# Kernel optimization log

Hardware: AMD Instinct MI355X
Metric: run time of the kernel (lower is better)

The kernel has to match this reference:

```python
import jax, jax.numpy as jnp
import numpy as np

N_NODES = 50000
N_EDGES = 1600000  # even; edges come in reverse pairs (i, i^1)
D_NODE = 128
D_EDGE = 32
UNITS = 128
STEPS = 4


def setup_inputs() -> dict:
    key = jax.random.key(0)
    ks = jax.random.split(key, 8)
    # Build directed edges as adjacent reverse pairs so rev(e) = e XOR 1.
    half = N_EDGES // 2
    src = jax.random.randint(ks[0], (half,), 0, N_NODES, dtype=jnp.int32)
    dst = jax.random.randint(ks[1], (half,), 0, N_NODES, dtype=jnp.int32)
    edge_src = jnp.stack([src, dst], axis=1).reshape(-1)
    edge_dst = jnp.stack([dst, src], axis=1).reshape(-1)
    node_feature = jax.random.normal(ks[2], (N_NODES, D_NODE), dtype=jnp.float32)
    edge_feature = jax.random.normal(ks[3], (N_EDGES, D_EDGE), dtype=jnp.float32)
    s_i = 1.0 / np.sqrt(D_NODE + D_EDGE)
    s_u = 1.0 / np.sqrt(UNITS)
    s_f = 1.0 / np.sqrt(D_NODE + UNITS)
    Wi = jax.random.normal(ks[4], (D_NODE + D_EDGE, UNITS), dtype=jnp.float32) * s_i
    Wu = jax.random.normal(ks[5], (UNITS, UNITS), dtype=jnp.float32) * s_u
    Wf = jax.random.normal(ks[6], (D_NODE + UNITS, UNITS), dtype=jnp.float32) * s_f
    bi = jnp.zeros((UNITS,), jnp.float32)
    bu = jnp.zeros((UNITS,), jnp.float32)
    bf = jnp.zeros((UNITS,), jnp.float32)
    return {
        'node_feature': node_feature, 'edge_feature': edge_feature,
        'edge_src': edge_src, 'edge_dst': edge_dst,
        'Wi': Wi, 'bi': bi, 'Wu': Wu, 'bu': bu, 'Wf': Wf, 'bf': bf,
    }


def reference(node_feature, edge_feature, edge_src, edge_dst, Wi, bi, Wu, bu, Wf, bf):
    n_nodes = node_feature.shape[0]
    n_edges = edge_src.shape[0]
    # reverse edge of e is e XOR 1 (edges built as adjacent pairs)
    rev = jnp.bitwise_xor(jnp.arange(n_edges, dtype=jnp.int32), 1)

    # initial projection: relu([x_src || e] Wi + bi)  -> [E, UNITS]
    h = jax.nn.relu(
        jnp.concatenate([node_feature[edge_src], edge_feature], axis=-1) @ Wi + bi)

    for _ in range(STEPS):
        # aggregate incoming edge states at each node, gather at edge_src,
        # subtract the reverse edge state (DMPNN message)
        agg = jax.ops.segment_sum(h, edge_dst, num_segments=n_nodes)  # [N, UNITS]
        message = agg[edge_src] - h[rev]                              # [E, UNITS]
        h = jax.nn.relu(message @ Wu + bu + h)

    node_message = jax.ops.segment_sum(h, edge_dst, num_segments=n_nodes)
    out = jax.nn.relu(
        jnp.concatenate([node_feature, node_message], axis=-1) @ Wf + bf)
    return out
```

## Files before the change

kernel.cpp:

```cpp
#include <hip/hip_runtime.h>
#include <hip/hip_bf16.h>

#define N_NODES 50000
#define N_EDGES 1600000
#define TILE    128

typedef __bf16 bf16x8 __attribute__((ext_vector_type(8)));
typedef __bf16 bf16x4 __attribute__((ext_vector_type(4)));
typedef float  f32x4  __attribute__((ext_vector_type(4)));

static __device__ __forceinline__ bf16x8 ld8(const __bf16* p) {
  return *reinterpret_cast<const bf16x8*>(p);
}
static __device__ __forceinline__ void st8(__bf16* p, bf16x8 v) {
  *reinterpret_cast<bf16x8*>(p) = v;
}

static __device__ __forceinline__ void async16(const void* g, void* l) {
  auto gp = (const __attribute__((address_space(1))) unsigned int*)(unsigned long long)g;
  auto lp = (__attribute__((address_space(3))) unsigned int*)(unsigned int)(unsigned long long)l;
  __builtin_amdgcn_global_load_lds(gp, lp, 16, 0, 0);
}

__global__ __launch_bounds__(256) void k_prep_w(
    const float* __restrict__ Wi, const float* __restrict__ Wu,
    const float* __restrict__ Wf,
    __bf16* __restrict__ WiT, __bf16* __restrict__ WuT, __bf16* __restrict__ WfT)
{
  int g = blockIdx.x * 256 + threadIdx.x;
  if (g < 160 * 128) {
    int n = g / 160, k = g % 160;
    WiT[g] = (__bf16)Wi[k * 128 + n];
  } else if (g < 160 * 128 + 128 * 128) {
    int gg = g - 160 * 128;
    int n = gg / 128, k = gg % 128;
    WuT[gg] = (__bf16)Wu[k * 128 + n];
  } else if (g < 160 * 128 + 128 * 128 + 256 * 128) {
    int gg = g - (160 * 128 + 128 * 128);
    int n = gg / 256, k = gg % 256;
    WfT[gg] = (__bf16)Wf[k * 128 + n];
  }
}

__global__ __launch_bounds__(256) void k_cvt(
    const float* __restrict__ in, __bf16* __restrict__ out, long n)
{
  long i = ((long)blockIdx.x * 256 + threadIdx.x) * 8;
  if (i + 8 <= n) {
    f32x4 f0 = *(const f32x4*)(in + i);
    f32x4 f1 = *(const f32x4*)(in + i + 4);
    bf16x8 o;
#pragma unroll
    for (int j = 0; j < 4; ++j) { o[j] = (__bf16)f0[j]; o[4 + j] = (__bf16)f1[j]; }
    st8(out + i, o);
  }
}

__global__ __launch_bounds__(256) void k_hist(
    const int* __restrict__ edst, int* __restrict__ cnt)
{
  int e = blockIdx.x * 256 + threadIdx.x;
  if (e < N_EDGES) atomicAdd(&cnt[edst[e]], 1);
}

__global__ __launch_bounds__(1024) void k_scan1(
    int* __restrict__ cnt, int* __restrict__ bsum, int n)
{
  __shared__ int sm[1024];
  const int tid = threadIdx.x;
  int i = blockIdx.x * 1024 + tid;
  int v = (i < n) ? cnt[i] : 0;
  sm[tid] = v;
  __syncthreads();
  for (int off = 1; off < 1024; off <<= 1) {
    int t = (tid >= off) ? sm[tid - off] : 0;
    __syncthreads();
    sm[tid] += t;
    __syncthreads();
  }
  if (i < n) cnt[i] = sm[tid] - v;
  if (tid == 1023) bsum[blockIdx.x] = sm[1023];
}

__global__ __launch_bounds__(64) void k_scan2(int* __restrict__ bsum, int nb)
{
  if (threadIdx.x == 0) {
    int acc = 0;
    for (int k = 0; k < nb; ++k) { int t = bsum[k]; bsum[k] = acc; acc += t; }
  }
}

__global__ __launch_bounds__(256) void k_scan3(
    const int* __restrict__ cnt, const int* __restrict__ bsum,
    int* __restrict__ cursor, int n)
{
  int i = blockIdx.x * 256 + threadIdx.x;
  if (i < n) cursor[i] = cnt[i] + bsum[i >> 10];
}

__global__ __launch_bounds__(256) void k_fill(
    const int* __restrict__ edst, int* __restrict__ cursor, int* __restrict__ eidx)
{
  int e = blockIdx.x * 256 + threadIdx.x;
  if (e < N_EDGES) {
    int p = atomicAdd(&cursor[edst[e]], 1);
    eidx[p] = e;
  }
}

__global__ __launch_bounds__(256) void k_agg(
    const __bf16* __restrict__ h, const int* __restrict__ cnt,
    const int* __restrict__ bsum, const int* __restrict__ eidx,
    const __bf16* __restrict__ zrow, __bf16* __restrict__ aggbf)
{
  const int wave = threadIdx.x >> 6;
  const int node = blockIdx.x * 4 + wave;
  const int lane = threadIdx.x & 63;
  const int g = lane >> 3, c8 = lane & 7;
  const int s = cnt[node] + bsum[node >> 10];
  const int e = (node + 1 < N_NODES) ? (cnt[node + 1] + bsum[(node + 1) >> 10]) : N_EDGES;
  const int deg = e - s;

  float a[16] = {};
  if (deg > 0) {
    const int* bucket = eidx + s;
    const int nit = (deg + 7) >> 3;
    int j0 = g;
    int e0 = bucket[(j0 < deg) ? j0 : 0];
    int e1 = bucket[(j0 + 8 < deg) ? j0 + 8 : 0];
    bool v0 = (j0 < deg), v1 = (j0 + 8 < deg);
    const __bf16* p0 = v0 ? (h + (long)e0 * 128 + c8 * 16) : zrow;
    bf16x8 r0 = ld8(p0), r1 = ld8(p0 + 8);
    for (int it = 0; it < nit; ++it) {
      const int j2 = j0 + 16;
      const int e2 = bucket[(j2 < deg) ? j2 : 0];
      const __bf16* p1 = v1 ? (h + (long)e1 * 128 + c8 * 16) : zrow;
      bf16x8 n0 = ld8(p1), n1 = ld8(p1 + 8);
#pragma unroll
      for (int k = 0; k < 8; ++k) {
        a[k]     += (float)r0[k];
        a[8 + k] += (float)r1[k];
      }
      r0 = n0; r1 = n1;
      e1 = e2; v1 = (j2 < deg);
      j0 += 8;
    }
  }
#pragma unroll
  for (int k = 0; k < 16; ++k) {
    a[k] += __shfl_xor(a[k], 8, 64);
    a[k] += __shfl_xor(a[k], 16, 64);
    a[k] += __shfl_xor(a[k], 32, 64);
  }
  if (g == 0) {
    bf16x8 o0, o1;
#pragma unroll
    for (int k = 0; k < 8; ++k) { o0[k] = (__bf16)a[k]; o1[k] = (__bf16)a[8 + k]; }
    st8(aggbf + (long)node * 128 + c8 * 16, o0);
    st8(aggbf + (long)node * 128 + c8 * 16 + 8, o1);
  }
}

__global__ __launch_bounds__(256) void k_nodegemm(
    const __bf16* __restrict__ A, const __bf16* __restrict__ BT, const int ldb,
    const float* __restrict__ bias, __bf16* __restrict__ outb, const int nrows)
{
  const int tid = threadIdx.x;
  const int lane = tid & 63, wave = tid >> 6;
  const int l15 = lane & 15, quad = lane >> 4;
  const int wm = wave >> 1, wn = wave & 1;
  const int base = blockIdx.x * TILE;

  int rowm[4];
#pragma unroll
  for (int ms = 0; ms < 4; ++ms) {
    int nd = base + wm * 64 + ms * 16 + l15;
    rowm[ms] = nd < nrows ? nd : (nrows - 1);
  }
  f32x4 acc[4][4] = {};
#pragma unroll
  for (int kit = 0; kit < 4; ++kit) {
    const int koff = kit * 32 + quad * 8;
    bf16x8 b[4];
#pragma unroll
    for (int ms = 0; ms < 4; ++ms)
      b[ms] = ld8(A + (long)rowm[ms] * 128 + koff);
#pragma unroll
    for (int ns = 0; ns < 4; ++ns) {
      bf16x8 a = ld8(BT + (wn * 64 + ns * 16 + l15) * ldb + koff);
#pragma unroll
      for (int ms = 0; ms < 4; ++ms)
        acc[ms][ns] = __builtin_amdgcn_mfma_f32_16x16x32_bf16(a, b[ms], acc[ms][ns], 0, 0, 0);
    }
  }
#pragma unroll
  for (int ns = 0; ns < 4; ++ns) {
    const int col = wn * 64 + ns * 16 + quad * 4;
    const f32x4 bv = *(const f32x4*)(bias + col);
#pragma unroll
    for (int ms = 0; ms < 4; ++ms) {
      const int node = base + wm * 64 + ms * 16 + l15;
      if (node < nrows) {
        bf16x4 o;
#pragma unroll
        for (int j = 0; j < 4; ++j) o[j] = (__bf16)(acc[ms][ns][j] + bv[j]);
        *(bf16x4*)(outb + (long)node * 128 + col) = o;
      }
    }
  }
}

__global__ __launch_bounds__(512) void k_init(
    const float* __restrict__ ef, const int* __restrict__ esrc,
    const __bf16* __restrict__ WiT, const __bf16* __restrict__ q,
    __bf16* __restrict__ h)
{
  __shared__ __align__(16) __bf16 cbuf[128 * 128];
  const int tid = threadIdx.x;
  const int lane = tid & 63, wave = tid >> 6;
  const int l15 = lane & 15, quad = lane >> 4;
  const int wm = wave >> 2, wn = wave & 3;
  const long base = (long)blockIdx.x * TILE;

  const int c15 = tid & 15, rbase = tid >> 4;
  int srcv[4];
#pragma unroll
  for (int i = 0; i < 4; ++i) srcv[i] = esrc[base + i * 32 + rbase];
  bf16x8 gp[4];
#pragma unroll
  for (int i = 0; i < 4; ++i) gp[i] = ld8(q + (long)srcv[i] * 128 + c15 * 8);

  f32x4 acc[4][2] = {};
  {
    bf16x8 a[4];
#pragma unroll
    for (int ms = 0; ms < 4; ++ms) {
      const int rm = wm * 64 + ms * 16 + l15;
      f32x4 f0 = *(const f32x4*)(ef + (base + rm) * 32 + quad * 8);
      f32x4 f1 = *(const f32x4*)(ef + (base + rm) * 32 + quad * 8 + 4);
      bf16x8 v;
#pragma unroll
      for (int j = 0; j < 4; ++j) { v[j] = (__bf16)f0[j]; v[4 + j] = (__bf16)f1[j]; }
      a[ms] = v;
    }
#pragma unroll
    for (int ns = 0; ns < 2; ++ns) {
      bf16x8 b = ld8(WiT + (wn * 32 + ns * 16 + l15) * 160 + 128 + quad * 8);
#pragma unroll
      for (int ms = 0; ms < 4; ++ms)
        acc[ms][ns] = __builtin_amdgcn_mfma_f32_16x16x32_bf16(a[ms], b, acc[ms][ns], 0, 0, 0);
    }
  }

#pragma unroll
  for (int ns = 0; ns < 2; ++ns) {
    const int col = wn * 32 + ns * 16 + l15;
#pragma unroll
    for (int ms = 0; ms < 4; ++ms) {
      const int r0 = wm * 64 + ms * 16 + quad * 4;
#pragma unroll
      for (int r = 0; r < 4; ++r) {
        const int row = r0 + r;
        cbuf[row * 128 + (((col >> 3) ^ (row & 15)) * 8) + (col & 7)] = (__bf16)acc[ms][ns][r];
      }
    }
  }
  __syncthreads();

#pragma unroll
  for (int i = 0; i < 4; ++i) {
    const int row = i * 32 + rbase;
    bf16x8 cv = ld8(cbuf + row * 128 + ((c15 ^ (row & 15)) * 8));
    bf16x8 o;
#pragma unroll
    for (int j = 0; j < 8; ++j) {
      float v = (float)gp[i][j] + (float)cv[j];
      o[j] = (__bf16)(v > 0.f ? v : 0.f);
    }
    st8(h + (base + row) * 128 + c15 * 8, o);
  }
}

__global__ __launch_bounds__(512) void k_update(
    __bf16* __restrict__ h, const int* __restrict__ esrc,
    const __bf16* __restrict__ WuT, const __bf16* __restrict__ gW)
{
  __shared__ __align__(16) __bf16 smem[128 * 128];
  __shared__ __align__(16) __bf16 cbuf[128 * 128];
  const int tid = threadIdx.x;
  const int lane = tid & 63, wave = tid >> 6;
  const int l15 = lane & 15, quad = lane >> 4;
  const int wm = wave >> 2, wn = wave & 3;
  const long base = (long)blockIdx.x * TILE;

  const int c15 = tid & 15, rbase = tid >> 4;
  int srcv[4];
#pragma unroll
  for (int i = 0; i < 4; ++i) srcv[i] = esrc[base + i * 32 + rbase];

#pragma unroll
  for (int j = 0; j < 4; ++j) {
    const int r = wave * 16 + j * 4 + (lane >> 4);
    const int cd = (lane & 15) ^ (r & 15);
    async16(h + (base + r) * 128 + cd * 8, smem + (wave * 16 + j * 4) * 128);
  }

  bf16x8 gp[4];
#pragma unroll
  for (int i = 0; i < 4; ++i) gp[i] = ld8(gW + (long)srcv[i] * 128 + c15 * 8);

  __syncthreads();

  f32x4 acc[4][2] = {};
#pragma unroll
  for (int kit = 0; kit < 4; ++kit) {
    bf16x8 a[4];
#pragma unroll
    for (int ms = 0; ms < 4; ++ms) {
      const int rm = wm * 64 + ms * 16 + l15;
      a[ms] = ld8(smem + rm * 128 + (((kit * 4 + quad) ^ l15) * 8));
    }
#pragma unroll
    for (int ns = 0; ns < 2; ++ns) {
      bf16x8 b = ld8(WuT + (wn * 32 + ns * 16 + l15) * 128 + kit * 32 + quad * 8);
#pragma unroll
      for (int ms = 0; ms < 4; ++ms)
        acc[ms][ns] = __builtin_amdgcn_mfma_f32_16x16x32_bf16(a[ms], b, acc[ms][ns], 0, 0, 0);
    }
  }

#pragma unroll
  for (int ns = 0; ns < 2; ++ns) {
    const int col = wn * 32 + ns * 16 + l15;
#pragma unroll
    for (int ms = 0; ms < 4; ++ms) {
      const int r0 = wm * 64 + ms * 16 + quad * 4;
#pragma unroll
      for (int r = 0; r < 4; ++r) {
        const int row = r0 + r;
        cbuf[row * 128 + (((col >> 3) ^ (row & 15)) * 8) + (col & 7)] = (__bf16)acc[ms][ns][r];
      }
    }
  }
  __syncthreads();

#pragma unroll
  for (int i = 0; i < 4; ++i) {
    const int row = i * 32 + rbase;
    const int rowr = row ^ 1;
    bf16x8 cv = ld8(cbuf + rowr * 128 + ((c15 ^ (rowr & 15)) * 8));
    bf16x8 hv = ld8(smem + row * 128 + ((c15 ^ (row & 15)) * 8));
    bf16x8 o;
#pragma unroll
    for (int j = 0; j < 8; ++j) {
      float v = (float)gp[i][j] - (float)cv[j] + (float)hv[j];
      o[j] = (__bf16)(v > 0.f ? v : 0.f);
    }
    st8(h + (base + row) * 128 + c15 * 8, o);
  }
}

__global__ __launch_bounds__(256) void k_final(
    const __bf16* __restrict__ nfbf, const __bf16* __restrict__ aggbf,
    const __bf16* __restrict__ WfT, const float* __restrict__ bfb,
    float* __restrict__ out)
{
  const int tid = threadIdx.x;
  const int lane = tid & 63, wave = tid >> 6;
  const int l15 = lane & 15, quad = lane >> 4;
  const int wm = wave >> 1, wn = wave & 1;
  const int base = blockIdx.x * TILE;

  int rowm[4];
#pragma unroll
  for (int ms = 0; ms < 4; ++ms) {
    int nd = base + wm * 64 + ms * 16 + l15;
    rowm[ms] = nd < N_NODES ? nd : (N_NODES - 1);
  }
  f32x4 acc[4][4] = {};
#pragma unroll
  for (int kit = 0; kit < 8; ++kit) {
    const int koff = kit * 32 + quad * 8;
    bf16x8 b[4];
#pragma unroll
    for (int ms = 0; ms < 4; ++ms)
      b[ms] = (kit < 4) ? ld8(nfbf + (long)rowm[ms] * 128 + koff)
                        : ld8(aggbf + (long)rowm[ms] * 128 + (koff - 128));
#pragma unroll
    for (int ns = 0; ns < 4; ++ns) {
      bf16x8 a = ld8(WfT + (wn * 64 + ns * 16 + l15) * 256 + koff);
#pragma unroll
      for (int ms = 0; ms < 4; ++ms)
        acc[ms][ns] = __builtin_amdgcn_mfma_f32_16x16x32_bf16(a, b[ms], acc[ms][ns], 0, 0, 0);
    }
  }
#pragma unroll
  for (int ns = 0; ns < 4; ++ns) {
    const int col = wn * 64 + ns * 16 + quad * 4;
    const f32x4 bv = *(const f32x4*)(bfb + col);
#pragma unroll
    for (int ms = 0; ms < 4; ++ms) {
      const int node = base + wm * 64 + ms * 16 + l15;
      if (node < N_NODES) {
        f32x4 o;
#pragma unroll
        for (int j = 0; j < 4; ++j) {
          float v = acc[ms][ns][j] + bv[j];
          o[j] = v > 0.f ? v : 0.f;
        }
        *(f32x4*)(out + (long)node * 128 + col) = o;
      }
    }
  }
}

extern "C" void kernel_launch(void* const* d_in, const int* in_sizes, int n_in,
                              void* d_out, int out_size, void* d_ws, size_t ws_size,
                              hipStream_t stream) {
  const float* nf   = (const float*)d_in[0];
  const float* ef   = (const float*)d_in[1];
  const int*   esrc = (const int*)d_in[2];
  const int*   edst = (const int*)d_in[3];
  const float* Wi   = (const float*)d_in[4];
  const float* bi   = (const float*)d_in[5];
  const float* Wu   = (const float*)d_in[6];
  const float* bu   = (const float*)d_in[7];
  const float* Wf   = (const float*)d_in[8];
  const float* bfb  = (const float*)d_in[9];
  float* out = (float*)d_out;

  char* ws = (char*)d_ws;
  __bf16* h      = (__bf16*)(ws);
  __bf16* aggbf  = (__bf16*)(ws + 409600000L);
  __bf16* nfbf   = (__bf16*)(ws + 422400000L);
  __bf16* WiT    = (__bf16*)(ws + 435200000L);
  __bf16* WuT    = (__bf16*)(ws + 435240960L);
  __bf16* WfT    = (__bf16*)(ws + 435273728L);
  int*    cnt    = (int*)(ws + 435339264L);
  int*    cursor = (int*)(ws + 435539264L);
  int*    bsum   = (int*)(ws + 435739264L);
  int*    eidx   = (int*)(ws + 435739520L);
  __bf16* g      = (__bf16*)(ws + 442139520L);

  const long NV = (long)N_NODES * 128;
  const int  NGB = (N_NODES + TILE - 1) / TILE;

  hipLaunchKernelGGL(k_prep_w, dim3(272), dim3(256), 0, stream, Wi, Wu, Wf, WiT, WuT, WfT);
  hipLaunchKernelGGL(k_cvt, dim3(3125), dim3(256), 0, stream, nf, nfbf, NV);
  hipMemsetAsync(cnt, 0, 200000, stream);
  hipLaunchKernelGGL(k_hist, dim3(N_EDGES / 256), dim3(256), 0, stream, edst, cnt);
  hipLaunchKernelGGL(k_scan1, dim3(49), dim3(1024), 0, stream, cnt, bsum, N_NODES);
  hipLaunchKernelGGL(k_scan2, dim3(1), dim3(64), 0, stream, bsum, 49);
  hipLaunchKernelGGL(k_scan3, dim3(196), dim3(256), 0, stream, cnt, bsum, cursor, N_NODES);
  hipLaunchKernelGGL(k_fill, dim3(N_EDGES / 256), dim3(256), 0, stream, edst, cursor, eidx);
  hipMemsetAsync(cursor, 0, 256, stream);
  const __bf16* zrow = (const __bf16*)cursor;

  hipLaunchKernelGGL(k_nodegemm, dim3(NGB), dim3(256), 0, stream, nfbf, WiT, 160, bi, g, N_NODES);
  hipLaunchKernelGGL(k_init, dim3(N_EDGES / TILE), dim3(512), 0, stream, ef, esrc, WiT, g, h);

  for (int t = 0; t < 4; ++t) {
    hipLaunchKernelGGL(k_agg, dim3(N_NODES / 4), dim3(256), 0, stream, h, cnt, bsum, eidx, zrow, aggbf);
    hipLaunchKernelGGL(k_nodegemm, dim3(NGB), dim3(256), 0, stream, aggbf, WuT, 128, bu, g, N_NODES);
    hipLaunchKernelGGL(k_update, dim3(N_EDGES / TILE), dim3(512), 0, stream, h, esrc, WuT, g);
  }
  hipLaunchKernelGGL(k_agg, dim3(N_NODES / 4), dim3(256), 0, stream, h, cnt, bsum, eidx, zrow, aggbf);
  hipLaunchKernelGGL(k_final, dim3(NGB), dim3(256), 0, stream, nfbf, aggbf, WfT, bfb, out);
}
```

Before: 2.026 ms.

## Fuse message subtraction before Wu GEMM and drop per-step node GEMM

```diff
diff --git a/kernel.cpp b/kernel.cpp
--- a/kernel.cpp
+++ b/kernel.cpp
@@ -125,25 +125,28 @@
   if (deg > 0) {
     const int* bucket = eidx + s;
     const int nit = (deg + 7) >> 3;
-    int j0 = g;
-    int e0 = bucket[(j0 < deg) ? j0 : 0];
-    int e1 = bucket[(j0 + 8 < deg) ? j0 + 8 : 0];
-    bool v0 = (j0 < deg), v1 = (j0 + 8 < deg);
-    const __bf16* p0 = v0 ? (h + (long)e0 * 128 + c8 * 16) : zrow;
-    bf16x8 r0 = ld8(p0), r1 = ld8(p0 + 8);
+    int j = g;
+    int ea = bucket[(j      < deg) ? j      : 0]; bool va = (j      < deg);
+    int eb = bucket[(j + 8  < deg) ? j + 8  : 0]; bool vb = (j + 8  < deg);
+    int ec = bucket[(j + 16 < deg) ? j + 16 : 0]; bool vc = (j + 16 < deg);
+    const __bf16* pa = va ? (h + (long)ea * 128 + c8 * 16) : zrow;
+    bf16x8 r0a = ld8(pa), r0b = ld8(pa + 8);
+    const __bf16* pb = vb ? (h + (long)eb * 128 + c8 * 16) : zrow;
+    bf16x8 r1a = ld8(pb), r1b = ld8(pb + 8);
     for (int it = 0; it < nit; ++it) {
-      const int j2 = j0 + 16;
-      const int e2 = bucket[(j2 < deg) ? j2 : 0];
-      const __bf16* p1 = v1 ? (h + (long)e1 * 128 + c8 * 16) : zrow;
-      bf16x8 n0 = ld8(p1), n1 = ld8(p1 + 8);
+      const int jn = j + 24;
+      const int ed = bucket[(jn < deg) ? jn : 0]; const bool vd = (jn < deg);
+      const __bf16* pc = vc ? (h + (long)ec * 128 + c8 * 16) : zrow;
+      bf16x8 r2a = ld8(pc), r2b = ld8(pc + 8);
 #pragma unroll
       for (int k = 0; k < 8; ++k) {
-        a[k]     += (float)r0[k];
-        a[8 + k] += (float)r1[k];
+        a[k]     += (float)r0a[k];
+        a[8 + k] += (float)r0b[k];
       }
-      r0 = n0; r1 = n1;
-      e1 = e2; v1 = (j2 < deg);
-      j0 += 8;
+      r0a = r1a; r0b = r1b; r1a = r2a; r1b = r2b;
+      ea = eb; eb = ec; ec = ed;
+      va = vb; vb = vc; vc = vd;
+      j += 8;
     }
   }
 #pragma unroll
@@ -283,10 +286,11 @@
 
 __global__ __launch_bounds__(512) void k_update(
     __bf16* __restrict__ h, const int* __restrict__ esrc,
-    const __bf16* __restrict__ WuT, const __bf16* __restrict__ gW)
+    const __bf16* __restrict__ WuT, const float* __restrict__ bu,
+    const __bf16* __restrict__ agg)
 {
   __shared__ __align__(16) __bf16 smem[128 * 128];
-  __shared__ __align__(16) __bf16 cbuf[128 * 128];
+  __shared__ __align__(16) __bf16 dbuf[128 * 128];
   const int tid = threadIdx.x;
   const int lane = tid & 63, wave = tid >> 6;
   const int l15 = lane & 15, quad = lane >> 4;
@@ -307,56 +311,64 @@
 
   bf16x8 gp[4];
 #pragma unroll
-  for (int i = 0; i < 4; ++i) gp[i] = ld8(gW + (long)srcv[i] * 128 + c15 * 8);
-
-  __syncthreads();
-
-  f32x4 acc[4][2] = {};
-#pragma unroll
-  for (int kit = 0; kit < 4; ++kit) {
-    bf16x8 a[4];
-#pragma unroll
-    for (int ms = 0; ms < 4; ++ms) {
-      const int rm = wm * 64 + ms * 16 + l15;
-      a[ms] = ld8(smem + rm * 128 + (((kit * 4 + quad) ^ l15) * 8));
-    }
-#pragma unroll
-    for (int ns = 0; ns < 2; ++ns) {
-      bf16x8 b = ld8(WuT + (wn * 32 + ns * 16 + l15) * 128 + kit * 32 + quad * 8);
-#pragma unroll
-      for (int ms = 0; ms < 4; ++ms)
-        acc[ms][ns] = __builtin_amdgcn_mfma_f32_16x16x32_bf16(a[ms], b, acc[ms][ns], 0, 0, 0);
-    }
-  }
-
-#pragma unroll
-  for (int ns = 0; ns < 2; ++ns) {
-    const int col = wn * 32 + ns * 16 + l15;
-#pragma unroll
-    for (int ms = 0; ms < 4; ++ms) {
-      const int r0 = wm * 64 + ms * 16 + quad * 4;
-#pragma unroll
-      for (int r = 0; r < 4; ++r) {
-        const int row = r0 + r;
-        cbuf[row * 128 + (((col >> 3) ^ (row & 15)) * 8) + (col & 7)] = (__bf16)acc[ms][ns][r];
-      }
-    }
-  }
+  for (int i = 0; i < 4; ++i) gp[i] = ld8(agg + (long)srcv[i] * 128 + c15 * 8);
+
+  bf16x8 wfrag[4][2];
+#pragma unroll
+  for (int kit = 0; kit < 4; ++kit)
+#pragma unroll
+    for (int ns = 0; ns < 2; ++ns)
+      wfrag[kit][ns] = ld8(WuT + (wn * 32 + ns * 16 + l15) * 128 + kit * 32 + quad * 8);
+
   __syncthreads();
 
 #pragma unroll
   for (int i = 0; i < 4; ++i) {
     const int row = i * 32 + rbase;
     const int rowr = row ^ 1;
-    bf16x8 cv = ld8(cbuf + rowr * 128 + ((c15 ^ (rowr & 15)) * 8));
-    bf16x8 hv = ld8(smem + row * 128 + ((c15 ^ (row & 15)) * 8));
-    bf16x8 o;
-#pragma unroll
-    for (int j = 0; j < 8; ++j) {
-      float v = (float)gp[i][j] - (float)cv[j] + (float)hv[j];
-      o[j] = (__bf16)(v > 0.f ? v : 0.f);
-    }
-    st8(h + (base + row) * 128 + c15 * 8, o);
+    bf16x8 hr = ld8(smem + rowr * 128 + ((c15 ^ (rowr & 15)) * 8));
+    bf16x8 d;
+#pragma unroll
+    for (int j = 0; j < 8; ++j) d[j] = (__bf16)((float)gp[i][j] - (float)hr[j]);
+    st8(dbuf + row * 128 + ((c15 ^ (row & 15)) * 8), d);
+  }
+  __syncthreads();
+
+  f32x4 acc[4][2] = {};
+#pragma unroll
+  for (int kit = 0; kit < 4; ++kit) {
+    bf16x8 a[4];
+#pragma unroll
+    for (int ms = 0; ms < 4; ++ms) {
+      const int rm = wm * 64 + ms * 16 + l15;
+      a[ms] = ld8(dbuf + rm * 128 + (((kit * 4 + quad) ^ l15) * 8));
+    }
+#pragma unroll
+    for (int ns = 0; ns < 2; ++ns) {
+#pragma unroll
+      for (int ms = 0; ms < 4; ++ms)
+        acc[ms][ns] = __builtin_amdgcn_mfma_f32_16x16x32_bf16(wfrag[kit][ns], a[ms], acc[ms][ns], 0, 0, 0);
+    }
+  }
+
+#pragma unroll
+  for (int ns = 0; ns < 2; ++ns) {
+    const int col = wn * 32 + ns * 16 + quad * 4;
+    const f32x4 bv = *(const f32x4*)(bu + col);
+    const int ch = (col >> 3);
+#pragma unroll
+    for (int ms = 0; ms < 4; ++ms) {
+      const int row = wm * 64 + ms * 16 + l15;
+      const __bf16* rp = smem + row * 128 + ((ch ^ (row & 15)) * 8) + (col & 7);
+      bf16x4 hr4 = *(const bf16x4*)rp;
+      bf16x4 o;
+#pragma unroll
+      for (int j = 0; j < 4; ++j) {
+        float v = acc[ms][ns][j] + bv[j] + (float)hr4[j];
+        o[j] = (__bf16)(v > 0.f ? v : 0.f);
+      }
+      *(bf16x4*)(h + (base + row) * 128 + col) = o;
+    }
   }
 }
 
@@ -461,8 +473,7 @@
 
   for (int t = 0; t < 4; ++t) {
     hipLaunchKernelGGL(k_agg, dim3(N_NODES / 4), dim3(256), 0, stream, h, cnt, bsum, eidx, zrow, aggbf);
-    hipLaunchKernelGGL(k_nodegemm, dim3(NGB), dim3(256), 0, stream, aggbf, WuT, 128, bu, g, N_NODES);
-    hipLaunchKernelGGL(k_update, dim3(N_EDGES / TILE), dim3(512), 0, stream, h, esrc, WuT, g);
+    hipLaunchKernelGGL(k_update, dim3(N_EDGES / TILE), dim3(512), 0, stream, h, esrc, WuT, bu, aggbf);
   }
   hipLaunchKernelGGL(k_agg, dim3(N_NODES / 4), dim3(256), 0, stream, h, cnt, bsum, eidx, zrow, aggbf);
   hipLaunchKernelGGL(k_final, dim3(NGB), dim3(256), 0, stream, nfbf, aggbf, WfT, bfb, out);
```

New measurement: 2.206 ms. 1.09x slower.
